# Performance work log

Hardware: AMD Instinct MI355X
Metric: run time of the kernel (lower is better)

## Reference

```python
import jax, jax.numpy as jnp
import numpy as np

B, S, D = 16, 1024, 1024
E = 8            # num routed experts
I_MOE = 2048     # moe_intermediate_size
I_SH = 2048      # shared_expert_intermediate_size
TOP_K = 2
K_CAP = max(1, min(int(S / E * TOP_K), S))  # tokens kept per expert = 256
UNCOND_LABEL = 1000
INIT_STD = 0.02


def _l2norm(x, axis=-1, eps=1e-12):
    # matches F.normalize(p=2): x / max(||x||, eps)
    n = jnp.sqrt(jnp.sum(x * x, axis=axis, keepdims=True))
    return x / jnp.maximum(n, eps)


def _mlp(x, Wg, Wu, Wd):
    # gated SiLU MLP: down(silu(gate(x)) * up(x))
    return (jax.nn.silu(x @ Wg) * (x @ Wu)) @ Wd


def setup_inputs() -> dict:
    key = jax.random.key(0)
    ks = jax.random.split(key, 12)
    hidden_states = jax.random.normal(ks[0], (B, S, D), dtype=jnp.float32)
    labels = jax.random.randint(ks[1], (B,), 0, 1001, dtype=jnp.int64)
    cluster_centers = jax.random.normal(ks[2], (E, D), dtype=jnp.float32) * INIT_STD
    sc = 0.02
    # routed experts stacked along E
    Wg = jax.random.normal(ks[3], (E, D, I_MOE), dtype=jnp.float32) * sc
    Wu = jax.random.normal(ks[4], (E, D, I_MOE), dtype=jnp.float32) * sc
    Wd = jax.random.normal(ks[5], (E, I_MOE, D), dtype=jnp.float32) * sc
    # uncond expert (experts[-1])
    u_Wg = jax.random.normal(ks[6], (D, I_MOE), dtype=jnp.float32) * sc
    u_Wu = jax.random.normal(ks[7], (D, I_MOE), dtype=jnp.float32) * sc
    u_Wd = jax.random.normal(ks[8], (I_MOE, D), dtype=jnp.float32) * sc
    # shared expert
    s_Wg = jax.random.normal(ks[9], (D, I_SH), dtype=jnp.float32) * sc
    s_Wu = jax.random.normal(ks[10], (D, I_SH), dtype=jnp.float32) * sc
    s_Wd = jax.random.normal(ks[11], (I_SH, D), dtype=jnp.float32) * sc
    return dict(hidden_states=hidden_states, labels=labels,
                cluster_centers=cluster_centers, Wg=Wg, Wu=Wu, Wd=Wd,
                u_Wg=u_Wg, u_Wu=u_Wu, u_Wd=u_Wd,
                s_Wg=s_Wg, s_Wu=s_Wu, s_Wd=s_Wd)


def reference(hidden_states, labels, cluster_centers, Wg, Wu, Wd,
              u_Wg, u_Wu, u_Wd, s_Wg, s_Wu, s_Wd):
    Bc, Sc, Dc = hidden_states.shape
    # ---- router: cosine similarity, softmax over tokens, expert-choice top-k ----
    x_n = _l2norm(hidden_states)                 # (B,S,D)
    c_n = _l2norm(cluster_centers)               # (E,D)
    cos_sim = jnp.einsum('bsd,ed->bes', x_n, c_n)  # expert view (B,E,S)
    cond_weights = jax.nn.softmax(cos_sim, axis=-1)  # softmax over S
    gating, idx = jax.lax.top_k(cond_weights, K_CAP)  # (B,E,k) each; sums, so sort order irrelevant
    # ---- dispatch (gather replaces one-hot einsum) ----
    expert_inputs = jnp.take_along_axis(hidden_states[:, None, :, :],
                                        idx[..., None], axis=2)   # (B,E,k,D)
    # ---- per-expert gated MLP as grouped GEMM ----
    h = jax.nn.silu(jnp.einsum('bekd,edi->beki', expert_inputs, Wg)) * \
        jnp.einsum('bekd,edi->beki', expert_inputs, Wu)
    expert_outputs = jnp.einsum('beki,eid->bekd', h, Wd)          # (B,E,k,D)
    # ---- weighted combine (scatter-add replaces one-hot einsum) ----
    weighted = gating[..., None] * expert_outputs                  # (B,E,k,D)
    cond_output = jnp.zeros_like(hidden_states).at[
        jnp.arange(Bc)[:, None], idx.reshape(Bc, -1)
    ].add(weighted.reshape(Bc, -1, Dc))                            # (B,S,D)
    # ---- uncond expert path, selected per batch by label ----
    uncond_output = _mlp(hidden_states, u_Wg, u_Wu, u_Wd)
    cond_mask = (labels != UNCOND_LABEL)[:, None, None]
    final_output = jnp.where(cond_mask, cond_output, uncond_output)
    # ---- shared expert ----
    final_output = final_output + _mlp(hidden_states, s_Wg, s_Wu, s_Wd)
    return final_output
```

## Files before the change

### kernel.cpp

```cpp
#include <hip/hip_runtime.h>
#include <stdint.h>

typedef __bf16 bf16;
typedef __attribute__((ext_vector_type(8))) __bf16 bf16x8;
typedef __attribute__((ext_vector_type(4))) float f32x4;

__device__ __forceinline__ void async_copy16(void* lds, const void* gp) {
    __builtin_amdgcn_global_load_lds(
        (__attribute__((address_space(1))) void*)(gp),
        (__attribute__((address_space(3))) void*)(lds), 16, 0, 0);
}

__device__ __forceinline__ const bf16* lread(const bf16* base, int R, int lq) {
    return base + R * 32 + (((lq + (R >> 1)) & 3) << 3);
}

__device__ __forceinline__ void xcd_remap(int& bx, int& by, int& bz) {
    int gx = gridDim.x, gy = gridDim.y, gz = gridDim.z;
    int panels = gy * gz;
    if (panels & 7) { bx = blockIdx.x; by = blockIdx.y; bz = blockIdx.z; return; }
    int L = (blockIdx.z * gy + blockIdx.y) * gx + blockIdx.x;
    int X = L & 7, S = L >> 3;
    bx = S % gx;
    int P = S / gx;
    int byT = X * (panels >> 3) + P;
    bz = byT / gy;
    by = byT % gy;
}


__global__ __launch_bounds__(256) void cnorm_kernel(const float* __restrict__ centers,
                                                    float* __restrict__ invc) {
    int e = blockIdx.x, t = threadIdx.x;
    float4 v = ((const float4*)(centers + (size_t)e * 1024))[t];
    float ss = v.x * v.x + v.y * v.y + v.z * v.z + v.w * v.w;
    #pragma unroll
    for (int o = 32; o; o >>= 1) ss += __shfl_down(ss, o);
    __shared__ float red[4];
    if ((t & 63) == 0) red[t >> 6] = ss;
    __syncthreads();
    if (t == 0) invc[e] = 1.f / fmaxf(sqrtf(red[0] + red[1] + red[2] + red[3]), 1e-12f);
}

__global__ __launch_bounds__(256) void router_convert_kernel(
    const float* __restrict__ X, const float* __restrict__ centers,
    const float* __restrict__ invc, bf16* __restrict__ hid, float* __restrict__ P) {
    int tok = blockIdx.x, t = threadIdx.x;
    int b = tok >> 10, s = tok & 1023;
    float4 v = ((const float4*)(X + (size_t)tok * 1024))[t];
    union { bf16 h[4]; uint2 u; } cv;
    cv.h[0] = (bf16)v.x; cv.h[1] = (bf16)v.y; cv.h[2] = (bf16)v.z; cv.h[3] = (bf16)v.w;
    ((uint2*)(hid + (size_t)tok * 1024))[t] = cv.u;
    float ss = v.x * v.x + v.y * v.y + v.z * v.z + v.w * v.w;
    float dots[8];
    #pragma unroll
    for (int e = 0; e < 8; e++) {
        float4 c = ((const float4*)(centers + (size_t)e * 1024))[t];
        dots[e] = v.x * c.x + v.y * c.y + v.z * c.z + v.w * c.w;
    }
    #pragma unroll
    for (int o = 32; o; o >>= 1) {
        ss += __shfl_down(ss, o);
        #pragma unroll
        for (int e = 0; e < 8; e++) dots[e] += __shfl_down(dots[e], o);
    }
    __shared__ float red[4][9];
    if ((t & 63) == 0) {
        red[t >> 6][0] = ss;
        #pragma unroll
        for (int e = 0; e < 8; e++) red[t >> 6][1 + e] = dots[e];
    }
    __syncthreads();
    if (t < 8) {
        float S = red[0][0] + red[1][0] + red[2][0] + red[3][0];
        float rinv = 1.f / fmaxf(sqrtf(S), 1e-12f);
        float d = red[0][1 + t] + red[1][1 + t] + red[2][1 + t] + red[3][1 + t];
        P[((size_t)(b * 8 + t) << 10) + s] = d * rinv * invc[t];
    }
}

__global__ __launch_bounds__(256) void softmax_kernel(float* __restrict__ P) {
    int row = blockIdx.x, t = threadIdx.x;
    float4* p4 = (float4*)(P + ((size_t)row << 10));
    float4 v = p4[t];
    float mx = fmaxf(fmaxf(v.x, v.y), fmaxf(v.z, v.w));
    #pragma unroll
    for (int o = 32; o; o >>= 1) mx = fmaxf(mx, __shfl_down(mx, o));
    __shared__ float red[8];
    if ((t & 63) == 0) red[t >> 6] = mx;
    __syncthreads();
    float M = fmaxf(fmaxf(red[0], red[1]), fmaxf(red[2], red[3]));
    float e0 = expf(v.x - M), e1 = expf(v.y - M), e2 = expf(v.z - M), e3 = expf(v.w - M);
    float s = e0 + e1 + e2 + e3;
    #pragma unroll
    for (int o = 32; o; o >>= 1) s += __shfl_down(s, o);
    if ((t & 63) == 0) red[4 + (t >> 6)] = s;
    __syncthreads();
    float inv = 1.f / (red[4] + red[5] + red[6] + red[7]);
    p4[t] = make_float4(e0 * inv, e1 * inv, e2 * inv, e3 * inv);
}

__global__ __launch_bounds__(256) void zero_cnt_kernel(int* __restrict__ cnt) {
    cnt[blockIdx.x * 256 + threadIdx.x] = 0;
}

__global__ __launch_bounds__(1024) void topk_kernel(const float* __restrict__ P,
                                                    int* __restrict__ row_map,
                                                    float* __restrict__ gsc,
                                                    int* __restrict__ cnt,
                                                    int* __restrict__ inv) {
    int row = blockIdx.x, t = threadIdx.x;
    __shared__ unsigned long long keys[1024];
    float v = P[((size_t)row << 10) + t];
    unsigned u = __float_as_uint(v);
    u = (u & 0x80000000u) ? ~u : (u | 0x80000000u);
    keys[t] = ((unsigned long long)u << 32) | (unsigned)(~t);
    __syncthreads();
    for (int k = 2; k <= 1024; k <<= 1) {
        for (int j = k >> 1; j > 0; j >>= 1) {
            int ixj = t ^ j;
            if (ixj > t) {
                bool up = ((t & k) == 0);
                unsigned long long a = keys[t], b = keys[ixj];
                if ((a > b) == up) { keys[t] = b; keys[ixj] = a; }
            }
            __syncthreads();
        }
    }
    if (t >= 768) {
        int slot = t - 768;
        int s = (int)(~(unsigned)keys[t]) & 1023;
        int b = row >> 3, e = row & 7;
        int m = e * 4096 + b * 256 + slot;
        int tok = b * 1024 + s;
        row_map[m] = tok;
        gsc[m] = P[((size_t)row << 10) + s];
        int pos = atomicAdd(cnt + tok, 1);
        inv[tok * 8 + pos] = m;
    }
}


__global__ __launch_bounds__(256) void transpose_cvt(
    const float* __restrict__ srcA, bf16* __restrict__ dstA, int batchA,
    const float* __restrict__ srcB, bf16* __restrict__ dstB, int R, int C) {
    int z = blockIdx.z;
    const float* src; bf16* dst;
    if (z < batchA) { src = srcA + (size_t)z * R * C; dst = dstA + (size_t)z * R * C; }
    else            { src = srcB + (size_t)(z - batchA) * R * C; dst = dstB + (size_t)(z - batchA) * R * C; }
    __shared__ float tile[32][33];
    int tx = threadIdx.x & 31, ty = threadIdx.x >> 5;
    int c0 = blockIdx.x * 32, r0 = blockIdx.y * 32;
    #pragma unroll
    for (int p = 0; p < 4; p++) {
        int r = p * 8 + ty;
        tile[r][tx] = src[(size_t)(r0 + r) * C + c0 + tx];
    }
    __syncthreads();
    #pragma unroll
    for (int p = 0; p < 4; p++) {
        int cl = p * 8 + ty;
        dst[(size_t)(c0 + cl) * R + r0 + tx] = (bf16)tile[tx][cl];
    }
}



__global__ __launch_bounds__(512) void gateup_kernel(
    const bf16* __restrict__ X, const int* __restrict__ row_map,
    const bf16* __restrict__ WgT, const bf16* __restrict__ WuT,
    bf16* __restrict__ H, int Mz, int m_base, const int* __restrict__ labels, int mode) {
    int bx, by, z; xcd_remap(bx, by, z);
    if (mode == 1) { int b = (m_base + by * 256) >> 10; if (labels[b] != 1000) return; }
    if (mode == 2) { int b = (m_base + by * 256) >> 8;  if (labels[b] == 1000) return; }
    __shared__ bf16 lds[2 * 16384];
    const int t = threadIdx.x;
    const bf16* Wg_e = WgT + (size_t)z * 2048 * 1024;
    const bf16* Wu_e = WuT + (size_t)z * 2048 * 1024;
    bf16* H_e = H + (size_t)z * Mz * 2048;

    const int m0 = by * 256, n0 = bx * 128;
    const int r = t >> 2;
    const int ce = (((t & 3) - (t >> 3)) & 3) * 8;
    int tok0, tok1;
    if (mode == 2) {
        const int* rm = row_map + (size_t)z * Mz;
        tok0 = rm[m0 + r]; tok1 = rm[m0 + 128 + r];
    } else { tok0 = m_base + m0 + r; tok1 = m_base + m0 + 128 + r; }
    const bf16* pa0 = X + (size_t)tok0 * 1024 + ce;
    const bf16* pa1 = X + (size_t)tok1 * 1024 + ce;
    const bf16* pg  = Wg_e + (size_t)(n0 + r) * 1024 + ce;
    const bf16* pu  = Wu_e + (size_t)(n0 + r) * 1024 + ce;

    const int l = t & 63, w = t >> 6;
    const int wm = w >> 2, wn = w & 3;
    const int lr = l & 15, lq = l >> 4;

    f32x4 accg[8][2] = {}, accu[8][2] = {};

    auto STAGE = [&](int s) {
        bf16* L = lds + s * 16384;
        async_copy16(L + t * 8, pa0);
        async_copy16(L + 4096 + t * 8, pa1);
        async_copy16(L + 8192 + t * 8, pg);
        async_copy16(L + 12288 + t * 8, pu);
        pa0 += 32; pa1 += 32; pg += 32; pu += 32;
    };

    const int NT = 1024 / 32;
    STAGE(0);
    __syncthreads();
    int cur = 0;
    for (int kt = 0; kt < NT; ++kt) {
        if (kt + 1 < NT) STAGE(cur ^ 1);
        const bf16* As = lds + cur * 16384;
        const bf16* Bg = As + 8192;
        const bf16* Bu = As + 12288;
        bf16x8 a[8], bg[2], bu[2];
        #pragma unroll
        for (int mi = 0; mi < 8; mi++)
            a[mi] = *(const bf16x8*)lread(As, wm * 128 + mi * 16 + lr, lq);
        #pragma unroll
        for (int ni = 0; ni < 2; ni++) {
            bg[ni] = *(const bf16x8*)lread(Bg, wn * 32 + ni * 16 + lr, lq);
            bu[ni] = *(const bf16x8*)lread(Bu, wn * 32 + ni * 16 + lr, lq);
        }
        #pragma unroll
        for (int mi = 0; mi < 8; mi++)
            #pragma unroll
            for (int ni = 0; ni < 2; ni++) {
                accg[mi][ni] = __builtin_amdgcn_mfma_f32_16x16x32_bf16(a[mi], bg[ni], accg[mi][ni], 0, 0, 0);
                accu[mi][ni] = __builtin_amdgcn_mfma_f32_16x16x32_bf16(a[mi], bu[ni], accu[mi][ni], 0, 0, 0);
            }
        __syncthreads();
        cur ^= 1;
    }
    #pragma unroll
    for (int mi = 0; mi < 8; mi++)
        #pragma unroll
        for (int ni = 0; ni < 2; ni++)
            #pragma unroll
            for (int rr = 0; rr < 4; rr++) {
                int m = m0 + wm * 128 + mi * 16 + lq * 4 + rr;
                int n = n0 + wn * 32 + ni * 16 + lr;
                float g = accg[mi][ni][rr], uu = accu[mi][ni][rr];
                float h = g / (1.f + __expf(-g)) * uu;
                H_e[(size_t)m * 2048 + n] = (bf16)h;
            }
}


__global__ __launch_bounds__(512) void down_kernel(
    const bf16* __restrict__ Hbase, const bf16* __restrict__ WdT,
    float* __restrict__ out, bf16* __restrict__ stage, int Mz, int m_base,
    const int* __restrict__ row_map, const float* __restrict__ gsc,
    const int* __restrict__ labels, int mode) {
    int bx, by, z; xcd_remap(bx, by, z);
    if (mode == 1) { int b = (m_base + by * 256) >> 10; if (labels[b] != 1000) return; }
    if (mode >= 2) { int b = (m_base + by * 256) >> 8;  if (labels[b] == 1000) return; }
    __shared__ bf16 lds[2 * 16384];
    const int t = threadIdx.x;
    const bf16* A_e = Hbase + (size_t)z * Mz * 2048;
    const bf16* B_e = WdT + (size_t)z * 1024 * 2048;
    const int m0 = by * 256, n0 = bx * 256;
    const int r = t >> 2;
    const int ce = (((t & 3) - (t >> 3)) & 3) * 8;
    const bf16* pa0 = A_e + (size_t)(m0 + r) * 2048 + ce;
    const bf16* pa1 = A_e + (size_t)(m0 + 128 + r) * 2048 + ce;
    const bf16* pb0 = B_e + (size_t)(n0 + r) * 2048 + ce;
    const bf16* pb1 = B_e + (size_t)(n0 + 128 + r) * 2048 + ce;

    const int l = t & 63, w = t >> 6;
    const int wm = w >> 2, wn = w & 3;
    const int lr = l & 15, lq = l >> 4;

    f32x4 acc[8][4] = {};

    auto STAGE = [&](int s) {
        bf16* L = lds + s * 16384;
        async_copy16(L + t * 8, pa0);
        async_copy16(L + 4096 + t * 8, pa1);
        async_copy16(L + 8192 + t * 8, pb0);
        async_copy16(L + 12288 + t * 8, pb1);
        pa0 += 32; pa1 += 32; pb0 += 32; pb1 += 32;
    };

    const int NT = 2048 / 32;
    STAGE(0);
    __syncthreads();
    int cur = 0;
    for (int kt = 0; kt < NT; ++kt) {
        if (kt + 1 < NT) STAGE(cur ^ 1);
        const bf16* As = lds + cur * 16384;
        const bf16* Bs = As + 8192;
        bf16x8 a[8], bb[4];
        #pragma unroll
        for (int mi = 0; mi < 8; mi++)
            a[mi] = *(const bf16x8*)lread(As, wm * 128 + mi * 16 + lr, lq);
        #pragma unroll
        for (int ni = 0; ni < 4; ni++)
            bb[ni] = *(const bf16x8*)lread(Bs, wn * 64 + ni * 16 + lr, lq);
        #pragma unroll
        for (int mi = 0; mi < 8; mi++)
            #pragma unroll
            for (int ni = 0; ni < 4; ni++)
                acc[mi][ni] = __builtin_amdgcn_mfma_f32_16x16x32_bf16(a[mi], bb[ni], acc[mi][ni], 0, 0, 0);
        __syncthreads();
        cur ^= 1;
    }
    float gs[8][4];
    if (mode >= 2) {
        #pragma unroll
        for (int mi = 0; mi < 8; mi++)
            #pragma unroll
            for (int rr = 0; rr < 4; rr++)
                gs[mi][rr] = gsc[(size_t)z * Mz + m0 + wm * 128 + mi * 16 + lq * 4 + rr];
    }
    #pragma unroll
    for (int mi = 0; mi < 8; mi++)
        #pragma unroll
        for (int ni = 0; ni < 4; ni++)
            #pragma unroll
            for (int rr = 0; rr < 4; rr++) {
                int m = m0 + wm * 128 + mi * 16 + lq * 4 + rr;
                int n = n0 + wn * 64 + ni * 16 + lr;
                float v = acc[mi][ni][rr];
                if (mode == 0) {
                    out[(size_t)(m_base + m) * 1024 + n] = v;
                } else if (mode == 1) {
                    out[(size_t)(m_base + m) * 1024 + n] += v;
                } else if (mode == 2) {
                    size_t em = (size_t)z * Mz + m;
                    stage[em * 1024 + n] = (bf16)(v * gs[mi][rr]);
                } else {
                    size_t em = (size_t)z * Mz + m;
                    int tok = row_map[em];
                    atomicAdd(out + (size_t)tok * 1024 + n, v * gs[mi][rr]);
                }
            }
}


__global__ __launch_bounds__(256) void combine_kernel(
    const bf16* __restrict__ stage, const int* __restrict__ cnt,
    const int* __restrict__ inv, const int* __restrict__ labels,
    float* __restrict__ out) {
    int tok = blockIdx.x;
    if (labels[tok >> 10] == 1000) return;
    int c = cnt[tok];
    if (c == 0) return;
    int t = threadIdx.x;
    float4* o4 = (float4*)(out + (size_t)tok * 1024);
    float4 acc = o4[t];
    for (int i = 0; i < c; i++) {
        int m = inv[tok * 8 + i];
        ushort4 raw = *(const ushort4*)(stage + (size_t)m * 1024 + t * 4);
        acc.x += __uint_as_float((unsigned)raw.x << 16);
        acc.y += __uint_as_float((unsigned)raw.y << 16);
        acc.z += __uint_as_float((unsigned)raw.z << 16);
        acc.w += __uint_as_float((unsigned)raw.w << 16);
    }
    o4[t] = acc;
}


extern "C" void kernel_launch(void* const* d_in, const int* in_sizes, int n_in,
                              void* d_out, int out_size, void* d_ws, size_t ws_size,
                              hipStream_t stream) {
    (void)in_sizes; (void)n_in; (void)out_size;
    const float* X       = (const float*)d_in[0];
    const int*   labels  = (const int*)d_in[1];
    const float* centers = (const float*)d_in[2];
    const float* Wg  = (const float*)d_in[3];
    const float* Wu  = (const float*)d_in[4];
    const float* Wd  = (const float*)d_in[5];
    const float* uWg = (const float*)d_in[6];
    const float* uWu = (const float*)d_in[7];
    const float* uWd = (const float*)d_in[8];
    const float* sWg = (const float*)d_in[9];
    const float* sWu = (const float*)d_in[10];
    const float* sWd = (const float*)d_in[11];
    float* out = (float*)d_out;

    char* w = (char*)d_ws;
    auto alloc = [&](size_t n) { char* p = w; w += (n + 255) & ~(size_t)255; return p; };
    bf16* hid  = (bf16*)alloc((size_t)16384 * 1024 * 2);
    bf16* WgT  = (bf16*)alloc((size_t)8 * 2048 * 1024 * 2);
    bf16* WuT  = (bf16*)alloc((size_t)8 * 2048 * 1024 * 2);
    bf16* WdT  = (bf16*)alloc((size_t)8 * 2048 * 1024 * 2);
    bf16* uWgT = (bf16*)alloc((size_t)2048 * 1024 * 2);
    bf16* uWuT = (bf16*)alloc((size_t)2048 * 1024 * 2);
    bf16* uWdT = (bf16*)alloc((size_t)2048 * 1024 * 2);
    bf16* sWgT = (bf16*)alloc((size_t)2048 * 1024 * 2);
    bf16* sWuT = (bf16*)alloc((size_t)2048 * 1024 * 2);
    bf16* sWdT = (bf16*)alloc((size_t)2048 * 1024 * 2);
    float* P     = (float*)alloc((size_t)128 * 1024 * 4);
    float* invc  = (float*)alloc(256);
    int*   rmap  = (int*)alloc((size_t)32768 * 4);
    float* gsc   = (float*)alloc((size_t)32768 * 4);
    int*   cnt   = (int*)alloc((size_t)16384 * 4);
    int*   inv   = (int*)alloc((size_t)16384 * 8 * 4);

    size_t used0 = (size_t)(w - (char*)d_ws);
    size_t rem0  = ws_size > used0 ? ws_size - used0 : 0;
    const size_t STAGE_BYTES = (size_t)32768 * 1024 * 2;
    const size_t HMIN_BYTES  = (size_t)8192 * 2048 * 2;
    bf16* stage = nullptr;
    if (rem0 >= STAGE_BYTES + HMIN_BYTES)
        stage = (bf16*)alloc(STAGE_BYTES);

    size_t used = (size_t)(w - (char*)d_ws);
    size_t hcap = ws_size > used ? ws_size - used : 0;
    bf16* H = (bf16*)w;
    long maxRows = (long)(hcap / ((size_t)2048 * 2));
    int CR = (int)(maxRows < 16384 ? maxRows : 16384);
    CR &= ~255;
    if (CR < 256) CR = 256;
    int EPG = 0;
    if (maxRows >= 32768) EPG = 8;
    else if (maxRows >= 16384) EPG = 4;
    else if (maxRows >= 8192)  EPG = 2;
    else if (maxRows >= 4096)  EPG = 1;

    const size_t WSTRIDE = (size_t)2048 * 1024;
    const int rmode = stage ? 2 : 3;

    cnorm_kernel<<<8, 256, 0, stream>>>(centers, invc);
    router_convert_kernel<<<16384, 256, 0, stream>>>(X, centers, invc, hid, P);
    softmax_kernel<<<128, 256, 0, stream>>>(P);
    zero_cnt_kernel<<<64, 256, 0, stream>>>(cnt);
    topk_kernel<<<128, 1024, 0, stream>>>(P, rmap, gsc, cnt, inv);
    transpose_cvt<<<dim3(64, 32, 16), 256, 0, stream>>>(Wg, WgT, 8, Wu, WuT, 1024, 2048);
    transpose_cvt<<<dim3(32, 64, 8), 256, 0, stream>>>(Wd, WdT, 8, nullptr, nullptr, 2048, 1024);
    transpose_cvt<<<dim3(64, 32, 2), 256, 0, stream>>>(uWg, uWgT, 1, sWg, sWgT, 1024, 2048);
    transpose_cvt<<<dim3(64, 32, 2), 256, 0, stream>>>(uWu, uWuT, 1, sWu, sWuT, 1024, 2048);
    transpose_cvt<<<dim3(32, 64, 2), 256, 0, stream>>>(uWd, uWdT, 1, sWd, sWdT, 2048, 1024);

    for (int m0 = 0; m0 < 16384; m0 += CR) {
        int rows = (16384 - m0 < CR) ? 16384 - m0 : CR;
        gateup_kernel<<<dim3(16, rows / 256, 1), 512, 0, stream>>>(
            hid, nullptr, sWgT, sWuT, H, rows, m0, labels, 0);
        down_kernel<<<dim3(4, rows / 256, 1), 512, 0, stream>>>(
            H, sWdT, out, nullptr, rows, m0, nullptr, nullptr, labels, 0);
    }
    for (int m0 = 0; m0 < 16384; m0 += CR) {
        int rows = (16384 - m0 < CR) ? 16384 - m0 : CR;
        gateup_kernel<<<dim3(16, rows / 256, 1), 512, 0, stream>>>(
            hid, nullptr, uWgT, uWuT, H, rows, m0, labels, 1);
        down_kernel<<<dim3(4, rows / 256, 1), 512, 0, stream>>>(
            H, uWdT, out, nullptr, rows, m0, nullptr, nullptr, labels, 1);
    }
    if (EPG > 0) {
        for (int g = 0; g < 8; g += EPG) {
            gateup_kernel<<<dim3(16, 16, EPG), 512, 0, stream>>>(
                hid, rmap + (size_t)g * 4096, WgT + (size_t)g * WSTRIDE,
                WuT + (size_t)g * WSTRIDE, H, 4096, 0, labels, 2);
            down_kernel<<<dim3(4, 16, EPG), 512, 0, stream>>>(
                H, WdT + (size_t)g * WSTRIDE, out,
                stage ? stage + (size_t)g * 4096 * 1024 : nullptr, 4096, 0,
                rmap + (size_t)g * 4096, gsc + (size_t)g * 4096, labels, rmode);
        }
    } else {
        for (int e = 0; e < 8; e++) {
            for (int m0 = 0; m0 < 4096; m0 += CR) {
                int rows = (4096 - m0 < CR) ? 4096 - m0 : CR;
                gateup_kernel<<<dim3(16, rows / 256, 1), 512, 0, stream>>>(
                    hid, rmap + (size_t)e * 4096 + m0, WgT + (size_t)e * WSTRIDE,
                    WuT + (size_t)e * WSTRIDE, H, rows, m0, labels, 2);
                down_kernel<<<dim3(4, rows / 256, 1), 512, 0, stream>>>(
                    H, WdT + (size_t)e * WSTRIDE, out,
                    stage ? stage + ((size_t)e * 4096 + m0) * 1024 : nullptr, rows, m0,
                    rmap + (size_t)e * 4096 + m0, gsc + (size_t)e * 4096 + m0, labels, rmode);
            }
        }
    }
    if (stage)
        combine_kernel<<<16384, 256, 0, stream>>>(stage, cnt, inv, labels, out);
}
```

Measured before the change: 1.098 ms.

## Deepen gate-up and down GEMM LDS pipeline to four stages with vmcnt waits

```diff
diff --git a/kernel.cpp b/kernel.cpp
--- a/kernel.cpp
+++ b/kernel.cpp
@@ -26,6 +26,14 @@
     int byT = X * (panels >> 3) + P;
     bz = byT / gy;
     by = byT % gy;
+}
+
+#define VMW(n) asm volatile("s_waitcnt vmcnt(" #n ")" ::: "memory")
+
+__device__ __forceinline__ void pipe_fence_pre()  { __builtin_amdgcn_sched_barrier(0); }
+__device__ __forceinline__ void pipe_fence_post() {
+    __builtin_amdgcn_s_barrier();
+    __builtin_amdgcn_sched_barrier(0);
 }
 
 
@@ -173,7 +181,7 @@
     int bx, by, z; xcd_remap(bx, by, z);
     if (mode == 1) { int b = (m_base + by * 256) >> 10; if (labels[b] != 1000) return; }
     if (mode == 2) { int b = (m_base + by * 256) >> 8;  if (labels[b] == 1000) return; }
-    __shared__ bf16 lds[2 * 16384];
+    __shared__ bf16 lds[4 * 16384];
     const int t = threadIdx.x;
     const bf16* Wg_e = WgT + (size_t)z * 2048 * 1024;
     const bf16* Wu_e = WuT + (size_t)z * 2048 * 1024;
@@ -208,12 +216,14 @@
     };
 
     const int NT = 1024 / 32;
-    STAGE(0);
-    __syncthreads();
-    int cur = 0;
-    for (int kt = 0; kt < NT; ++kt) {
-        if (kt + 1 < NT) STAGE(cur ^ 1);
-        const bf16* As = lds + cur * 16384;
+    STAGE(0); STAGE(1); STAGE(2);
+    VMW(8);
+    __builtin_amdgcn_s_barrier();
+    __builtin_amdgcn_sched_barrier(0);
+
+    for (int j = 0; j < NT; ++j) {
+        if (j + 3 < NT) STAGE((j + 3) & 3);
+        const bf16* As = lds + (j & 3) * 16384;
         const bf16* Bg = As + 8192;
         const bf16* Bu = As + 12288;
         bf16x8 a[8], bg[2], bu[2];
@@ -232,8 +242,13 @@
                 accg[mi][ni] = __builtin_amdgcn_mfma_f32_16x16x32_bf16(a[mi], bg[ni], accg[mi][ni], 0, 0, 0);
                 accu[mi][ni] = __builtin_amdgcn_mfma_f32_16x16x32_bf16(a[mi], bu[ni], accu[mi][ni], 0, 0, 0);
             }
-        __syncthreads();
-        cur ^= 1;
+        if (j + 1 < NT) {
+            pipe_fence_pre();
+            if (j + 3 < NT)      { VMW(8); }
+            else if (j + 2 < NT) { VMW(4); }
+            else                 { VMW(0); }
+            pipe_fence_post();
+        }
     }
     #pragma unroll
     for (int mi = 0; mi < 8; mi++)
@@ -258,7 +273,7 @@
     int bx, by, z; xcd_remap(bx, by, z);
     if (mode == 1) { int b = (m_base + by * 256) >> 10; if (labels[b] != 1000) return; }
     if (mode >= 2) { int b = (m_base + by * 256) >> 8;  if (labels[b] == 1000) return; }
-    __shared__ bf16 lds[2 * 16384];
+    __shared__ bf16 lds[4 * 16384];
     const int t = threadIdx.x;
     const bf16* A_e = Hbase + (size_t)z * Mz * 2048;
     const bf16* B_e = WdT + (size_t)z * 1024 * 2048;
@@ -286,12 +301,14 @@
     };
 
     const int NT = 2048 / 32;
-    STAGE(0);
-    __syncthreads();
-    int cur = 0;
-    for (int kt = 0; kt < NT; ++kt) {
-        if (kt + 1 < NT) STAGE(cur ^ 1);
-        const bf16* As = lds + cur * 16384;
+    STAGE(0); STAGE(1); STAGE(2);
+    VMW(8);
+    __builtin_amdgcn_s_barrier();
+    __builtin_amdgcn_sched_barrier(0);
+
+    for (int j = 0; j < NT; ++j) {
+        if (j + 3 < NT) STAGE((j + 3) & 3);
+        const bf16* As = lds + (j & 3) * 16384;
         const bf16* Bs = As + 8192;
         bf16x8 a[8], bb[4];
         #pragma unroll
@@ -305,8 +322,13 @@
             #pragma unroll
             for (int ni = 0; ni < 4; ni++)
                 acc[mi][ni] = __builtin_amdgcn_mfma_f32_16x16x32_bf16(a[mi], bb[ni], acc[mi][ni], 0, 0, 0);
-        __syncthreads();
-        cur ^= 1;
+        if (j + 1 < NT) {
+            pipe_fence_pre();
+            if (j + 3 < NT)      { VMW(8); }
+            else if (j + 2 < NT) { VMW(4); }
+            else                 { VMW(0); }
+            pipe_fence_post();
+        }
     }
     float gs[8][4];
     if (mode >= 2) {
```

Result: no change. 1.080 ms (-1.6%).
